# Kernel optimization log

Measured on AMD Instinct MI355X. Metric: run time of the kernel, lower is better.

The kernel has to match this reference:

```python
import jax, jax.numpy as jnp
import numpy as np
import math

NUM_HEADS = 2


def setup_inputs() -> dict:
    key = jax.random.key(0)
    k1, k2, k3, k4 = jax.random.split(key, 4)
    B, S, E = 16, 2048, 8  # embed_dim == n_wires == 8 (required by module structure)
    x = jax.random.normal(k1, (B, S, E), dtype=jnp.float32)
    theta = jax.random.normal(k2, (E,), dtype=jnp.float32)          # trainable RX angles, one per wire
    w_out = jax.random.normal(k3, (E, E), dtype=jnp.float32) / math.sqrt(E)  # out_proj weight
    b_out = jax.random.normal(k4, (E,), dtype=jnp.float32) * 0.01   # out_proj bias
    return {"x": x, "theta": theta, "w_out": w_out, "b_out": b_out}


def reference(x, theta, w_out, b_out):
    B, S, E = x.shape
    H = NUM_HEADS
    dk = E // H
    # Quantum projection, analytic form: per-wire RX(x) then RX(theta) on |0>,
    # PauliZ expectation -> cos(x + theta). Same layer applied for q, k, v.
    q = jnp.cos(x + theta)              # [B, S, E]
    qh = q.reshape(B, S, H, dk).transpose(0, 2, 1, 3)  # [B, H, S, dk]; q == k == v
    scores = jnp.einsum('bhqd,bhkd->bhqk', qh, qh) / jnp.sqrt(jnp.float32(dk))
    attn = jax.nn.softmax(scores, axis=-1)             # dropout is identity in eval
    out = jnp.einsum('bhqk,bhkd->bhqd', attn, qh)      # [B, H, S, dk]
    out = out.transpose(0, 2, 1, 3).reshape(B, S, E)
    return out @ w_out.T + b_out
```

## Files before the change

kernel.cpp:

```cpp
#include <hip/hip_runtime.h>
#include <math.h>

#define BB 16
#define SS 2048
#define HH 2
#define ROWS_PER_BLOCK 128
#define THREADS1 512
#define KT 16
#define NITER (SS / KT)
#define KVT_STRIDE 2064

typedef _Float16 half8 __attribute__((ext_vector_type(8)));
typedef _Float16 half4h __attribute__((ext_vector_type(4)));
typedef _Float16 half2h __attribute__((ext_vector_type(2)));
typedef float floatx4 __attribute__((ext_vector_type(4)));

__device__ __forceinline__ float fast_exp2(float x) {
  return __builtin_amdgcn_exp2f(x);
}

__device__ __forceinline__ half2h pkrtz(float a, float b) {
#if defined(__has_builtin)
#if __has_builtin(__builtin_amdgcn_cvt_pkrtz)
  return __builtin_bit_cast(half2h, __builtin_amdgcn_cvt_pkrtz(a, b));
#else
  half2h r; r[0] = (_Float16)a; r[1] = (_Float16)b; return r;
#endif
#else
  half2h r; r[0] = (_Float16)a; r[1] = (_Float16)b; return r;
#endif
}

__global__ __launch_bounds__(THREADS1, 4)
void qattn_fused(const float* __restrict__ x,
                 const float* __restrict__ theta,
                 const float* __restrict__ w_out,
                 const float* __restrict__ b_out,
                 float* __restrict__ out) {
  __shared__ half8 s_keys[SS];
  __shared__ _Float16 s_kvT[5 * KVT_STRIDE];
  __shared__ float po[ROWS_PER_BLOCK * 6];

  const int bid = blockIdx.x;
  const int rb  = bid & 15;
  const int h   = (bid >> 4) & 1;
  const int b   = bid >> 5;
  const int t   = threadIdx.x;

  const float4 th = ((const float4*)theta)[h];
  const float4* xb = (const float4*)x;

  for (int s = t; s < SS; s += THREADS1) {
    float4 xr = xb[(size_t)(b * SS + s) * 2 + h];
    _Float16 c0 = (_Float16)__cosf(xr.x + th.x);
    _Float16 c1 = (_Float16)__cosf(xr.y + th.y);
    _Float16 c2 = (_Float16)__cosf(xr.z + th.z);
    _Float16 c3 = (_Float16)__cosf(xr.w + th.w);
    const _Float16 z = (_Float16)0.0f;
    half8 v = {c0, c1, c2, c3, z, z, z, z};
    s_keys[s] = v;
    s_kvT[0 * KVT_STRIDE + s] = c0;
    s_kvT[1 * KVT_STRIDE + s] = c1;
    s_kvT[2 * KVT_STRIDE + s] = c2;
    s_kvT[3 * KVT_STRIDE + s] = c3;
  }
  for (int i = t; i < KVT_STRIDE; i += THREADS1)
    s_kvT[4 * KVT_STRIDE + i] = (_Float16)1.0f;
  __syncthreads();

  const int lane = t & 63;
  const int wv   = t >> 6;
  const int quad = lane >> 4;
  const int l15  = lane & 15;

  const float KS  = 0.72134752044448170367f;
  const float scl = (lane < 16) ? KS : 0.0f;
  const int   qrow = rb * ROWS_PER_BLOCK + wv * 16 + l15;
  half4h rq = *(const half4h*)&s_keys[qrow];
  const _Float16 z = (_Float16)0.0f;
  half8 bq = {(_Float16)((float)rq[0] * scl), (_Float16)((float)rq[1] * scl),
              (_Float16)((float)rq[2] * scl), (_Float16)((float)rq[3] * scl),
              z, z, z, z};

  const _Float16* bbase = s_kvT + (l15 < 4 ? l15 : 4) * KVT_STRIDE + quad * 4;

  floatx4 o = {0.f, 0.f, 0.f, 0.f};
  const floatx4 zf = {0.f, 0.f, 0.f, 0.f};
  half8 apv = {z, z, z, z, z, z, z, z};

#pragma unroll 4
  for (int kt = 0; kt < NITER; ++kt) {
    half8 a = s_keys[kt * KT + l15];
    half4h bl = *(const half4h*)(bbase + kt * KT);
    half8 bpv = {bl[0], bl[1], bl[2], bl[3], z, z, z, z};

    floatx4 c = __builtin_amdgcn_mfma_f32_16x16x32_f16(a, bq, zf, 0, 0, 0);

    half2h p01 = pkrtz(fast_exp2(c[0]), fast_exp2(c[1]));
    half2h p23 = pkrtz(fast_exp2(c[2]), fast_exp2(c[3]));
    apv[0] = p01[0]; apv[1] = p01[1]; apv[2] = p23[0]; apv[3] = p23[1];

    o = __builtin_amdgcn_mfma_f32_16x16x32_f16(apv, bpv, o, 0, 0, 0);
  }

  if (l15 < 5) {
#pragma unroll
    for (int r = 0; r < 4; ++r)
      po[(wv * 16 + quad * 4 + r) * 6 + l15] = o[r];
  }
  __syncthreads();

  {
    const int row = t >> 2;
    const int ep  = (t & 3) * 2;
    const float* pr = po + row * 6;
    const float inv = 1.0f / pr[4];
    const float o0 = pr[0] * inv, o1 = pr[1] * inv,
                o2 = pr[2] * inv, o3 = pr[3] * inv;
    float* op = out + ((size_t)(b * SS + rb * ROWS_PER_BLOCK + row)) * 8;
#pragma unroll
    for (int k = 0; k < 2; ++k) {
      const int e = ep + k;
      const float* wr = w_out + e * 8 + h * 4;
      float val = fmaf(o0, wr[0], fmaf(o1, wr[1], fmaf(o2, wr[2], o3 * wr[3])));
      if (h == 0) val += b_out[e];
      atomicAdd(op + e, val);
    }
  }
}

extern "C" void kernel_launch(void* const* d_in, const int* in_sizes, int n_in,
                              void* d_out, int out_size, void* d_ws, size_t ws_size,
                              hipStream_t stream) {
  const float* x     = (const float*)d_in[0];
  const float* theta = (const float*)d_in[1];
  const float* w_out = (const float*)d_in[2];
  const float* b_out = (const float*)d_in[3];
  float* out = (float*)d_out;
  (void)in_sizes; (void)n_in; (void)d_ws; (void)ws_size;

  (void)hipMemsetAsync(d_out, 0, (size_t)out_size * sizeof(float), stream);
  qattn_fused<<<dim3(BB * HH * 16), THREADS1, 0, stream>>>(x, theta, w_out, b_out, out);
}
```

Before: 81.01 us.

## Process two query tiles per wave so each key tile load feeds two MFMAs

Halves the block to 4 waves and has each wave handle 32 query rows as two 16-row MFMA tiles. Each loaded key and value tile is then reused for both query tiles, cutting LDS reads per unit of work and giving two independent MFMA chains to overlap with the exp work. The key array is shrunk to half4 in LDS and widened to half8 in registers. In exchange there are fewer waves per block and more register pressure, and the LDS staging prologue is spread over fewer threads.

```diff
diff --git a/kernel.cpp b/kernel.cpp
--- a/kernel.cpp
+++ b/kernel.cpp
@@ -5,7 +5,7 @@
 #define SS 2048
 #define HH 2
 #define ROWS_PER_BLOCK 128
-#define THREADS1 512
+#define THREADS1 256
 #define KT 16
 #define NITER (SS / KT)
 #define KVT_STRIDE 2064
@@ -31,13 +31,13 @@
 #endif
 }
 
-__global__ __launch_bounds__(THREADS1, 4)
+__global__ __launch_bounds__(THREADS1, 2)
 void qattn_fused(const float* __restrict__ x,
                  const float* __restrict__ theta,
                  const float* __restrict__ w_out,
                  const float* __restrict__ b_out,
                  float* __restrict__ out) {
-  __shared__ half8 s_keys[SS];
+  __shared__ half4h s_keys[SS];
   __shared__ _Float16 s_kvT[5 * KVT_STRIDE];
   __shared__ float po[ROWS_PER_BLOCK * 6];
 
@@ -56,8 +56,7 @@
     _Float16 c1 = (_Float16)__cosf(xr.y + th.y);
     _Float16 c2 = (_Float16)__cosf(xr.z + th.z);
     _Float16 c3 = (_Float16)__cosf(xr.w + th.w);
-    const _Float16 z = (_Float16)0.0f;
-    half8 v = {c0, c1, c2, c3, z, z, z, z};
+    half4h v = {c0, c1, c2, c3};
     s_keys[s] = v;
     s_kvT[0 * KVT_STRIDE + s] = c0;
     s_kvT[1 * KVT_STRIDE + s] = c1;
@@ -75,54 +74,69 @@
 
   const float KS  = 0.72134752044448170367f;
   const float scl = (lane < 16) ? KS : 0.0f;
-  const int   qrow = rb * ROWS_PER_BLOCK + wv * 16 + l15;
-  half4h rq = *(const half4h*)&s_keys[qrow];
+  const int   qrow = rb * ROWS_PER_BLOCK + wv * 32 + l15;
+  half4h rq0 = s_keys[qrow];
+  half4h rq1 = s_keys[qrow + 16];
   const _Float16 z = (_Float16)0.0f;
-  half8 bq = {(_Float16)((float)rq[0] * scl), (_Float16)((float)rq[1] * scl),
-              (_Float16)((float)rq[2] * scl), (_Float16)((float)rq[3] * scl),
-              z, z, z, z};
+  half8 bq0 = {(_Float16)((float)rq0[0] * scl), (_Float16)((float)rq0[1] * scl),
+               (_Float16)((float)rq0[2] * scl), (_Float16)((float)rq0[3] * scl),
+               z, z, z, z};
+  half8 bq1 = {(_Float16)((float)rq1[0] * scl), (_Float16)((float)rq1[1] * scl),
+               (_Float16)((float)rq1[2] * scl), (_Float16)((float)rq1[3] * scl),
+               z, z, z, z};
 
   const _Float16* bbase = s_kvT + (l15 < 4 ? l15 : 4) * KVT_STRIDE + quad * 4;
 
-  floatx4 o = {0.f, 0.f, 0.f, 0.f};
+  floatx4 o0 = {0.f, 0.f, 0.f, 0.f};
+  floatx4 o1 = {0.f, 0.f, 0.f, 0.f};
   const floatx4 zf = {0.f, 0.f, 0.f, 0.f};
-  half8 apv = {z, z, z, z, z, z, z, z};
+  half8 apv0 = {z, z, z, z, z, z, z, z};
+  half8 apv1 = {z, z, z, z, z, z, z, z};
 
 #pragma unroll 4
   for (int kt = 0; kt < NITER; ++kt) {
-    half8 a = s_keys[kt * KT + l15];
+    half4h al = s_keys[kt * KT + l15];
+    half8 a = {al[0], al[1], al[2], al[3], z, z, z, z};
     half4h bl = *(const half4h*)(bbase + kt * KT);
     half8 bpv = {bl[0], bl[1], bl[2], bl[3], z, z, z, z};
 
-    floatx4 c = __builtin_amdgcn_mfma_f32_16x16x32_f16(a, bq, zf, 0, 0, 0);
+    floatx4 c0 = __builtin_amdgcn_mfma_f32_16x16x32_f16(a, bq0, zf, 0, 0, 0);
+    floatx4 c1 = __builtin_amdgcn_mfma_f32_16x16x32_f16(a, bq1, zf, 0, 0, 0);
 
-    half2h p01 = pkrtz(fast_exp2(c[0]), fast_exp2(c[1]));
-    half2h p23 = pkrtz(fast_exp2(c[2]), fast_exp2(c[3]));
-    apv[0] = p01[0]; apv[1] = p01[1]; apv[2] = p23[0]; apv[3] = p23[1];
+    half2h p01 = pkrtz(fast_exp2(c0[0]), fast_exp2(c0[1]));
+    half2h p23 = pkrtz(fast_exp2(c0[2]), fast_exp2(c0[3]));
+    apv0[0] = p01[0]; apv0[1] = p01[1]; apv0[2] = p23[0]; apv0[3] = p23[1];
+    half2h p45 = pkrtz(fast_exp2(c1[0]), fast_exp2(c1[1]));
+    half2h p67 = pkrtz(fast_exp2(c1[2]), fast_exp2(c1[3]));
+    apv1[0] = p45[0]; apv1[1] = p45[1]; apv1[2] = p67[0]; apv1[3] = p67[1];
 
-    o = __builtin_amdgcn_mfma_f32_16x16x32_f16(apv, bpv, o, 0, 0, 0);
+    o0 = __builtin_amdgcn_mfma_f32_16x16x32_f16(apv0, bpv, o0, 0, 0, 0);
+    o1 = __builtin_amdgcn_mfma_f32_16x16x32_f16(apv1, bpv, o1, 0, 0, 0);
   }
 
   if (l15 < 5) {
 #pragma unroll
-    for (int r = 0; r < 4; ++r)
-      po[(wv * 16 + quad * 4 + r) * 6 + l15] = o[r];
+    for (int r = 0; r < 4; ++r) {
+      const int base = wv * 32 + quad * 4 + r;
+      po[base * 6 + l15]        = o0[r];
+      po[(base + 16) * 6 + l15] = o1[r];
+    }
   }
   __syncthreads();
 
   {
-    const int row = t >> 2;
-    const int ep  = (t & 3) * 2;
+    const int row = t >> 1;
+    const int ep  = (t & 1) * 4;
     const float* pr = po + row * 6;
     const float inv = 1.0f / pr[4];
-    const float o0 = pr[0] * inv, o1 = pr[1] * inv,
-                o2 = pr[2] * inv, o3 = pr[3] * inv;
+    const float o0v = pr[0] * inv, o1v = pr[1] * inv,
+                o2v = pr[2] * inv, o3v = pr[3] * inv;
     float* op = out + ((size_t)(b * SS + rb * ROWS_PER_BLOCK + row)) * 8;
 #pragma unroll
-    for (int k = 0; k < 2; ++k) {
+    for (int k = 0; k < 4; ++k) {
       const int e = ep + k;
       const float* wr = w_out + e * 8 + h * 4;
-      float val = fmaf(o0, wr[0], fmaf(o1, wr[1], fmaf(o2, wr[2], o3 * wr[3])));
+      float val = fmaf(o0v, wr[0], fmaf(o1v, wr[1], fmaf(o2v, wr[2], o3v * wr[3])));
       if (h == 0) val += b_out[e];
       atomicAdd(op + e, val);
     }
```

Result: slower. 84.27 us (+4.0%).
